# Kernel optimization log

Measured on AMD Instinct MI355X. Metric: run time of the kernel, lower is better.

The kernel has to match this reference:

```python
import jax, jax.numpy as jnp
import numpy as np

B, S, C = 2, 2048, 1536
HQ, HKV = 16, 4
DQK, DV = 128, 96
MAX_POS = 2048
CLIP = 5.0
EPS = 1e-5


def layer_norm(x, g, b):
    mu = jnp.mean(x, axis=-1, keepdims=True)
    var = jnp.mean(jnp.square(x - mu), axis=-1, keepdims=True)
    return (x - mu) * jax.lax.rsqrt(var + EPS) * g + b


def rms_bn(x, g, ms):
    # eval-mode EMA RMS batch-norm: per-channel running mean-square `ms`
    return x * jax.lax.rsqrt(ms + EPS) * g


def rope(x):
    # x: [B, S, H, C] with C even
    c = x.shape[-1]
    nf = c // 2
    s = x.shape[1]
    positions = jnp.arange(s, dtype=x.dtype)
    lin = jnp.arange(nf, dtype=x.dtype)
    end = max(MAX_POS - nf + 1.0, 1.0)
    geom = jnp.exp(jnp.linspace(0.0, jnp.log(jnp.asarray(end, dtype=x.dtype)), nf))
    inv_freq = 1.0 / (lin + geom)
    theta = positions[:, None] * inv_freq          # [S, nf]
    theta = jnp.repeat(theta, 2, axis=-1)[:, None, :]  # [S, 1, C]
    x_rot = jnp.stack([-x[..., 1::2], x[..., ::2]], axis=-1).reshape(x.shape)
    return x * jnp.cos(theta) + x_rot * jnp.sin(theta)


def setup_inputs() -> dict:
    key = jax.random.key(0)
    ks = jax.random.split(key, 8)
    d = {
        'x': jax.random.normal(ks[0], (B, S, C), dtype=jnp.float32),
        'bn1_g': jnp.ones((C,), jnp.float32),
        'bn1_ms': jnp.ones((C,), jnp.float32),
        'Wq': jax.random.normal(ks[1], (C, HQ * DQK), jnp.float32) * 0.02,
        'Wk': jax.random.normal(ks[2], (C, HKV * DQK), jnp.float32) * 0.02,
        'Wv': jax.random.normal(ks[3], (C, HKV * DV), jnp.float32) * 0.02,
        'qn_g': jnp.ones((DQK,), jnp.float32), 'qn_b': jnp.zeros((DQK,), jnp.float32),
        'kn_g': jnp.ones((DQK,), jnp.float32), 'kn_b': jnp.zeros((DQK,), jnp.float32),
        'vn_g': jnp.ones((DV,), jnp.float32), 'vn_b': jnp.zeros((DV,), jnp.float32),
        'Wo': jax.random.normal(ks[4], (HQ * DV, C), jnp.float32) * 0.02,
        'bo': jnp.zeros((C,), jnp.float32),
        'bn2_g': jnp.ones((C,), jnp.float32),
        'bn2_ms': jnp.ones((C,), jnp.float32),
    }
    return d


def reference(x, bn1_g, bn1_ms, Wq, Wk, Wv, qn_g, qn_b, kn_g, kn_b, vn_g, vn_b, Wo, bo, bn2_g, bn2_ms):
    rep = HQ // HKV
    h = rms_bn(x, bn1_g, bn1_ms)                       # [B,S,C]
    q = (h @ Wq).reshape(B, S, HQ, DQK)
    k = (h @ Wk).reshape(B, S, HKV, DQK)
    v = (h @ Wv).reshape(B, S, HKV, DV)
    q = layer_norm(q, qn_g, qn_b)
    k = layer_norm(k, kn_g, kn_b)
    v = layer_norm(v, vn_g, vn_b)
    q = rope(q)
    k = rope(k)
    # torch .repeat(1,1,rep,1) tiles head axis: [h0..hkv-1] * rep
    k = jnp.tile(k, (1, 1, rep, 1))                    # [B,S,HQ,DQK]
    v = jnp.tile(v, (1, 1, rep, 1))                    # [B,S,HQ,DV]
    logits = jnp.einsum('bshc,bShc->bhsS', q, k) / (DQK ** 0.5)
    logits = jnp.tanh(logits / CLIP) * CLIP
    attn = jax.nn.softmax(logits, axis=-1)
    y = jnp.einsum('bhsS,bShc->bshc', attn, v)         # [B,S,HQ,DV]
    y = y.reshape(B, S, HQ * DV)
    y = y @ Wo + bo
    y = rms_bn(y, bn2_g, bn2_ms)
    return y
```

## Files before the change

kernel.cpp:

```cpp
#include <hip/hip_runtime.h>
#include <hip/hip_bf16.h>
#include <math.h>

typedef __hip_bfloat16 bf16;
typedef __attribute__((ext_vector_type(8))) short short8;
typedef __attribute__((ext_vector_type(4))) short short4s;
typedef __attribute__((ext_vector_type(4))) float f32x4;

constexpr int Bb=2, Ss=2048, Cc=1536, HQn=16, HKVn=4, Dqk=128, Dv=96;
constexpr int NR   = Bb*Ss;
constexpr int NQKV = HQn*Dqk + HKVn*Dqk + HKVn*Dv;
constexpr int COL_K = HQn*Dqk;
constexpr int COL_V = COL_K + HKVn*Dqk;
constexpr int NY   = HQn*Dv;
constexpr float EPSf=1e-5f, CLIPf=5.0f;
constexpr float LOG2E = 1.44269504089f;

__device__ __forceinline__ float s2f(short s) {
    unsigned u = ((unsigned)(unsigned short)s) << 16;
    return __builtin_bit_cast(float, u);
}
__device__ __forceinline__ short f2s(float v) {
    bf16 b = __float2bfloat16(v);
    return __builtin_bit_cast(short, b);
}
__device__ __forceinline__ bool is_bf(const void* tagp) {
    return ((*(const unsigned*)tagp) & 0xFFFFu) != 0u;
}
__device__ __forceinline__ float ldd(const void* p, size_t i, bool bf) {
    return bf ? s2f(((const short*)p)[i]) : ((const float*)p)[i];
}
__device__ __forceinline__ void gll16(const void* src, void* lds) {
    __builtin_amdgcn_global_load_lds(
        (const __attribute__((address_space(1))) void*)src,
        (__attribute__((address_space(3))) void*)lds, 16, 0, 0);
}

__global__ __launch_bounds__(256) void k_pre(const void* g1, const void* ms1,
        const void* bo, const void* g2, const void* ms2,
        float* __restrict__ ascale, float* __restrict__ ebias,
        float* __restrict__ escale, float2* __restrict__ tab) {
    bool bf = is_bf(ms1);
    int idx = blockIdx.x*256 + threadIdx.x;
    if (idx < Cc) {
        ascale[idx] = rsqrtf(ldd(ms1,idx,bf) + EPSf) * ldd(g1,idx,bf);
        ebias[idx]  = ldd(bo,idx,bf);
        escale[idx] = rsqrtf(ldd(ms2,idx,bf) + EPSf) * ldd(g2,idx,bf);
    }
    if (idx < Ss*64) {
        int s = idx >> 6, f = idx & 63;
        float geom = expf((float)f * (logf(1985.0f) * (1.0f/63.0f)));
        float invf = 1.0f / ((float)f + geom);
        float th = (float)s * invf;
        tab[idx] = make_float2(cosf(th), sinf(th));
    }
}

__global__ __launch_bounds__(256) void k_bn1(const void* __restrict__ x,
        short* __restrict__ h, const void* tagp) {
    bool bf = is_bf(tagp);
    size_t i8 = (size_t)(blockIdx.x*256 + threadIdx.x) * 8;
    if (i8 >= (size_t)NR*Cc) return;
    if (bf) {
        *(short8*)(h + i8) = *(const short8*)((const short*)x + i8);
    } else {
        const float* xf = (const float*)x + i8;
        short8 o;
        #pragma unroll
        for (int j=0;j<8;++j) o[j] = f2s(xf[j]);
        *(short8*)(h + i8) = o;
    }
}

__global__ __launch_bounds__(256) void k_trw(const void* __restrict__ Wq,
        const void* __restrict__ Wk, const void* __restrict__ Wv,
        const void* __restrict__ Wo, short* __restrict__ WT,
        const float* __restrict__ ascale, const void* tagp) {
    __shared__ short tile[32][33];
    bool bf = is_bf(tagp);
    int gt = blockIdx.x*32;
    int k0 = blockIdx.y*32;
    const void* W; int N, nl;
    bool doscale = true;
    if      (gt < 2048) { W = Wq; N = 2048; nl = gt; }
    else if (gt < 2560) { W = Wk; N = 512;  nl = gt - 2048; }
    else if (gt < 2944) { W = Wv; N = 384;  nl = gt - 2560; }
    else                { W = Wo; N = 1536; nl = gt - 2944; doscale = false; }
    int t = threadIdx.x, c = t & 31;
    #pragma unroll
    for (int r8=0; r8<32; r8+=8) {
        int r = r8 + (t>>5);
        float sc = doscale ? ascale[k0+r] : 1.0f;
        tile[r][c] = f2s(ldd(W, (size_t)(k0+r)*N + nl + c, bf) * sc);
    }
    __syncthreads();
    #pragma unroll
    for (int r8=0; r8<32; r8+=8) {
        int r = r8 + (t>>5);
        WT[(size_t)(gt + r)*Cc + k0 + c] = tile[c][r];
    }
}

__global__ __launch_bounds__(256) void k_gemm(const short* __restrict__ A,
        const short* __restrict__ BT, void* __restrict__ Cout,
        int M, int N, int K,
        const float* __restrict__ ebias, const float* __restrict__ escale,
        int epi, const void* tagp) {
    __shared__ short As[128*32];
    __shared__ short Bs[128*32];
    const int t = threadIdx.x;
    const int w = t >> 6, lane = t & 63;
    const int l15 = lane & 15, quad = lane >> 4;
    const int wm = (w>>1)*64, wn = (w&1)*64;
    const int m0 = blockIdx.y*128, n0 = blockIdx.x*128;
    const int c0 = lane >> 2;
    const int koff = (lane & 3) * 8;

    f32x4 acc[4][4];
    #pragma unroll
    for (int i=0;i<4;++i)
        #pragma unroll
        for (int j=0;j<4;++j) acc[i][j] = (f32x4){0.f,0.f,0.f,0.f};

    for (int k0 = 0; k0 < K; k0 += 32) {
        __syncthreads();
        #pragma unroll
        for (int c=0; c<2; ++c) {
            int rA = w*32 + c*16;
            const short* ga = A  + (size_t)(m0 + rA + c0)*K + k0 + koff;
            const short* gb = BT + (size_t)(n0 + rA + c0)*K + k0 + koff;
            gll16(ga, &As[rA*32]);
            gll16(gb, &Bs[rA*32]);
        }
        __syncthreads();
        short8 af[4], bfr[4];
        #pragma unroll
        for (int mt=0; mt<4; ++mt)
            af[mt] = *(const short8*)&As[(wm + mt*16 + l15)*32 + quad*8];
        #pragma unroll
        for (int nt=0; nt<4; ++nt)
            bfr[nt] = *(const short8*)&Bs[(wn + nt*16 + l15)*32 + quad*8];
        #pragma unroll
        for (int mt=0; mt<4; ++mt)
            #pragma unroll
            for (int nt=0; nt<4; ++nt)
                acc[mt][nt] = __builtin_amdgcn_mfma_f32_16x16x32_bf16(
                    af[mt], bfr[nt], acc[mt][nt], 0, 0, 0);
    }

    const bool outf32 = epi && !is_bf(tagp);
    #pragma unroll
    for (int mt=0; mt<4; ++mt) {
        #pragma unroll
        for (int nt=0; nt<4; ++nt) {
            int col = n0 + wn + nt*16 + l15;
            float eb = epi ? ebias[col]  : 0.f;
            float es = epi ? escale[col] : 1.f;
            #pragma unroll
            for (int reg=0; reg<4; ++reg) {
                int row = m0 + wm + mt*16 + quad*4 + reg;
                float v = acc[mt][nt][reg];
                if (epi) v = (v + eb) * es;
                if (outf32) ((float*)Cout)[(size_t)row*N + col] = v;
                else        ((short*)Cout)[(size_t)row*N + col] = f2s(v);
            }
        }
    }
}

__global__ __launch_bounds__(512, 2) void k_gemm256(const short* __restrict__ A,
        const short* __restrict__ BT, short* __restrict__ Cout,
        int M, int Npad, int Nout, int K) {
    __shared__ __align__(16) short smem[4 * 2 * 256 * 32];
    const int t = threadIdx.x;
    const int w = t >> 6, lane = t & 63;
    const int wm = w >> 2, wn = w & 3;
    const int l15 = lane & 15, quad = lane >> 4;

    const int nwg = gridDim.x, cpx = nwg >> 3;
    const int swz = (blockIdx.x & 7)*cpx + (blockIdx.x >> 3);
    const int ntx = Npad >> 8;
    const int n0 = (swz % ntx) << 8, m0 = (swz / ntx) << 8;

    const int srow = lane >> 2;
    const int scol = (lane & 3) * 16;
    const short* Asrc = A  + (size_t)(m0 + srow)*K;
    const short* Bsrc = BT + (size_t)(n0 + srow)*K;

    f32x4 acc[8][4];
    #pragma unroll
    for (int i=0;i<8;++i)
        #pragma unroll
        for (int j=0;j<4;++j) acc[i][j] = (f32x4){0.f,0.f,0.f,0.f};

    const int H = K >> 5;
    auto stage = [&](int h) {
        const int slot = h & 3;
        char* AD = (char*)smem + slot*32768;
        char* BD = AD + 16384;
        const size_t koff = (size_t)h << 5;
        #pragma unroll
        for (int uu=0; uu<2; ++uu) {
            const int u = w + uu*8;
            const char* as = (const char*)(Asrc + (size_t)(u*16)*K + koff) + scol;
            const char* bs = (const char*)(Bsrc + (size_t)(u*16)*K + koff) + scol;
            gll16(as, AD + u*1024);
            gll16(bs, BD + u*1024);
        }
    };

    stage(0);
    if (H > 1) stage(1);
    if (H > 2) stage(2);

    for (int h = 0; h < H; ++h) {
        if (h+3 < H) stage(h+3);
        const int rem = H-1-h;
        if      (rem >= 3) asm volatile("s_waitcnt vmcnt(12)" ::: "memory");
        else if (rem == 2) asm volatile("s_waitcnt vmcnt(8)"  ::: "memory");
        else if (rem == 1) asm volatile("s_waitcnt vmcnt(4)"  ::: "memory");
        else               asm volatile("s_waitcnt vmcnt(0)"  ::: "memory");
        __builtin_amdgcn_s_barrier();

        const int slot = h & 3;
        const char* AD = (const char*)smem + slot*32768;
        const char* BD = AD + 16384;
        short8 af[8], bfr[4];
        #pragma unroll
        for (int i=0;i<8;++i) {
            int row = wm*128 + i*16 + l15;
            af[i] = *(const short8*)(AD + row*64 + quad*16);
        }
        #pragma unroll
        for (int j=0;j<4;++j) {
            int row = wn*64 + j*16 + l15;
            bfr[j] = *(const short8*)(BD + row*64 + quad*16);
        }
        asm volatile("s_waitcnt lgkmcnt(0)" ::: "memory");
        __builtin_amdgcn_sched_barrier(0);
        __builtin_amdgcn_s_setprio(1);
        #pragma unroll
        for (int i=0;i<8;++i)
            #pragma unroll
            for (int j=0;j<4;++j)
                acc[i][j] = __builtin_amdgcn_mfma_f32_16x16x32_bf16(
                    af[i], bfr[j], acc[i][j], 0, 0, 0);
        __builtin_amdgcn_s_setprio(0);
        __builtin_amdgcn_s_barrier();
    }

    #pragma unroll
    for (int mt=0; mt<8; ++mt) {
        #pragma unroll
        for (int nt=0; nt<4; ++nt) {
            int col = n0 + wn*64 + nt*16 + l15;
            if (col < Nout) {
                #pragma unroll
                for (int reg=0; reg<4; ++reg) {
                    int row = m0 + wm*128 + mt*16 + quad*4 + reg;
                    Cout[(size_t)row*Nout + col] = f2s(acc[mt][nt][reg]);
                }
            }
        }
    }
}

__global__ __launch_bounds__(256) void k_ln(short* __restrict__ qkvb,
        const float2* __restrict__ tab,
        const void* qg, const void* qb_, const void* kg, const void* kb_,
        const void* vg, const void* vb_, const void* tagp) {
    bool bf = is_bf(tagp);
    int R = blockIdx.x*4 + (threadIdx.x>>6);
    int lane = threadIdx.x & 63;
    int hidx = R % 24, bs = R / 24, s = bs % Ss;
    const void *g, *bia; int coff, D, dorope;
    if (hidx < 16)      { coff = hidx*Dqk;              D = Dqk; g = qg; bia = qb_; dorope = 1; }
    else if (hidx < 20) { coff = COL_K + (hidx-16)*Dqk; D = Dqk; g = kg; bia = kb_; dorope = 1; }
    else                { coff = COL_V + (hidx-20)*Dv;  D = Dv;  g = vg; bia = vb_; dorope = 0; }
    short* p = qkvb + (size_t)bs*NQKV + coff;
    int d0 = lane*2;
    bool act = d0 < D;
    float v0 = 0.f, v1 = 0.f;
    if (act) { v0 = s2f(p[d0]); v1 = s2f(p[d0+1]); }
    float sum = v0 + v1;
    #pragma unroll
    for (int m=1; m<64; m<<=1) sum += __shfl_xor(sum, m);
    float mu = sum / (float)D;
    float c0 = act ? v0-mu : 0.f, c1 = act ? v1-mu : 0.f;
    float sq = c0*c0 + c1*c1;
    #pragma unroll
    for (int m=1; m<64; m<<=1) sq += __shfl_xor(sq, m);
    float r = rsqrtf(sq/(float)D + EPSf);
    if (act) {
        float y0 = c0*r*ldd(g,d0,bf)   + ldd(bia,d0,bf);
        float y1 = c1*r*ldd(g,d0+1,bf) + ldd(bia,d0+1,bf);
        if (dorope) {
            float2 cs = tab[s*64 + lane];
            float t0 = y0*cs.x - y1*cs.y;
            y1 = y1*cs.x + y0*cs.y;
            y0 = t0;
        }
        p[d0] = f2s(y0); p[d0+1] = f2s(y1);
    }
}

__global__ __launch_bounds__(256) void k_trv(const short* __restrict__ qkvb,
        short* __restrict__ vT) {
    __shared__ short tile[32][33];
    int bs0 = blockIdx.x*32;
    int dg0 = blockIdx.y*32;
    int t = threadIdx.x, c = t & 31;
    #pragma unroll
    for (int r8=0; r8<32; r8+=8) {
        int r = r8 + (t>>5);
        tile[r][c] = qkvb[(size_t)(bs0+r)*NQKV + COL_V + dg0 + c];
    }
    __syncthreads();
    int b = bs0 >> 11, s0 = bs0 & 2047;
    int s = s0 + c;
    int sp = (s & ~63) + ((s>>5)&1)*32 + ((s>>2)&3)*8 + ((s>>4)&1)*4 + (s&3);
    #pragma unroll
    for (int r8=0; r8<32; r8+=8) {
        int r = r8 + (t>>5);
        vT[((size_t)(b*384 + dg0 + r))*Ss + sp] = tile[c][r];
    }
}

__global__ __launch_bounds__(512, 4) void k_attn(const short* __restrict__ qkvb,
        const short* __restrict__ vT, short* __restrict__ Yb) {
    __shared__ __align__(16) short smem[2*64*128 + 2*96*64];
    auto Ks  = (short(*)[64*128])smem;
    auto VTs = (short(*)[96*64])(smem + 2*64*128);
    const int wg = blockIdx.x;
    const int xcd = wg & 7, idx = wg >> 3;
    const int b = xcd >> 2, kvh = xcd & 3;
    const int qb = idx >> 2, hsub = idx & 3;
    const int hq = hsub*4 + kvh;
    const int q0 = qb*128;
    const int t = threadIdx.x;
    const int w = t >> 6, lane = t & 63;
    const int qw = w & 3, half = w >> 2;
    const int l15 = lane & 15, quad = lane >> 4;
    const int xr = (l15 & 7) * 16;
    const float ctan = 2.0f * (0.0883883476f / CLIPf) * LOG2E;
    const float c2   = -2.0f * CLIPf * LOG2E;

    const short* Kb = qkvb + ((size_t)b*Ss)*NQKV + COL_K + kvh*Dqk;
    const short* Vb = vT + ((size_t)(b*HKVn + kvh)*Dv)*Ss;

    const int rK = 4*w + (lane>>4);
    const char* kq0 = (const char*)Kb + (size_t)rK*NQKV*2
                    + (((lane&15)*16) ^ ((rK&7)*16));
    const int dv0 = 8*w + (lane>>3);
    const char* vq0 = (const char*)Vb + (size_t)dv0*Ss*2
                    + (((lane&7)*16) ^ ((dv0&7)*16));
    const size_t KADV = (size_t)64*NQKV*2;
    const size_t KOFF2 = (size_t)32*NQKV*2;
    const size_t VOFF2 = (size_t)64*Ss*2;

    auto issue_stage = [&](int pb) {
        char* KD = (char*)&Ks[pb][0];
        char* VD = (char*)&VTs[pb][0];
        gll16(kq0,         KD + w*1024);
        gll16(kq0 + KOFF2, KD + (w+8)*1024);
        gll16(vq0,         VD + w*1024);
        if (w < 4) gll16(vq0 + VOFF2, VD + (w+8)*1024);
        kq0 += KADV; vq0 += 128;
    };

    issue_stage(0);

    short8 qf[2][4];
    #pragma unroll
    for (int qt=0; qt<2; ++qt) {
        const short* qp = qkvb + (size_t)(b*Ss + q0 + qw*32 + qt*16 + l15)*NQKV + hq*Dqk;
        #pragma unroll
        for (int ds=0; ds<4; ++ds) qf[qt][ds] = *(const short8*)(qp + ds*32 + quad*8);
    }

    f32x4 oacc[2][6];
    #pragma unroll
    for (int qt=0; qt<2; ++qt)
        #pragma unroll
        for (int nt=0; nt<6; ++nt) oacc[qt][nt] = (f32x4){0.f,0.f,0.f,0.f};
    float lsum[2] = {0.f, 0.f};

    int p = 0;
    constexpr int NCH = Ss/64;
    for (int kc = 0; kc < NCH; ++kc) {
        __syncthreads();
        if (kc+1 < NCH) issue_stage(p^1);

        const char* KsB  = (const char*)&Ks[p][0];
        const char* VTsB = (const char*)&VTs[p][0];

        short8 pa[2];
        #pragma unroll
        for (int kt=0; kt<2; ++kt) {
            const int r = (half*2 + kt)*16 + l15;
            const char* krow = KsB + r*256;
            short8 kf[4];
            #pragma unroll
            for (int ds=0; ds<4; ++ds)
                kf[ds] = *(const short8*)(krow + ((ds*64 + quad*16) ^ xr));
            f32x4 s0 = (f32x4){0.f,0.f,0.f,0.f}, s1 = (f32x4){0.f,0.f,0.f,0.f};
            __builtin_amdgcn_s_setprio(1);
            #pragma unroll
            for (int ds=0; ds<4; ++ds) {
                s0 = __builtin_amdgcn_mfma_f32_16x16x32_bf16(kf[ds], qf[0][ds], s0, 0, 0, 0);
                s1 = __builtin_amdgcn_mfma_f32_16x16x32_bf16(kf[ds], qf[1][ds], s1, 0, 0, 0);
            }
            __builtin_amdgcn_s_setprio(0);
            #pragma unroll
            for (int j=0; j<4; ++j) {
                float u0 = __builtin_amdgcn_exp2f(s0[j] * ctan);
                float p0 = __builtin_amdgcn_exp2f(c2 * __builtin_amdgcn_rcpf(u0 + 1.0f));
                pa[0][kt*4+j] = f2s(p0); lsum[0] += p0;
                float u1 = __builtin_amdgcn_exp2f(s1[j] * ctan);
                float p1 = __builtin_amdgcn_exp2f(c2 * __builtin_amdgcn_rcpf(u1 + 1.0f));
                pa[1][kt*4+j] = f2s(p1); lsum[1] += p1;
            }
        }

        __builtin_amdgcn_s_setprio(1);
        #pragma unroll
        for (int nt=0; nt<6; ++nt) {
            const int dvrow = nt*16 + l15;
            short8 vf = *(const short8*)(VTsB + dvrow*128 + ((half*64 + quad*16) ^ xr));
            oacc[0][nt] = __builtin_amdgcn_mfma_f32_16x16x32_bf16(pa[0], vf, oacc[0][nt], 0, 0, 0);
            oacc[1][nt] = __builtin_amdgcn_mfma_f32_16x16x32_bf16(pa[1], vf, oacc[1][nt], 0, 0, 0);
        }
        __builtin_amdgcn_s_setprio(0);
        p ^= 1;
    }

    __syncthreads();
    float* red = (float*)smem;
    const int rbase = (qw*64 + lane)*53;
    if (half == 1) {
        #pragma unroll
        for (int qt=0; qt<2; ++qt)
            #pragma unroll
            for (int nt=0; nt<6; ++nt)
                *(f32x4*)&red[rbase + (qt*6+nt)*4] = oacc[qt][nt];
        red[rbase+48] = lsum[0];
        red[rbase+49] = lsum[1];
    }
    __syncthreads();
    if (half == 0) {
        #pragma unroll
        for (int qt=0; qt<2; ++qt)
            #pragma unroll
            for (int nt=0; nt<6; ++nt) {
                f32x4 o = *(const f32x4*)&red[rbase + (qt*6+nt)*4];
                #pragma unroll
                for (int j=0;j<4;++j) oacc[qt][nt][j] += o[j];
            }
        lsum[0] += red[rbase+48];
        lsum[1] += red[rbase+49];

        float lred[2];
        #pragma unroll
        for (int qt=0; qt<2; ++qt) {
            float l = lsum[qt];
            l += __shfl_xor(l, 16);
            l += __shfl_xor(l, 32);
            lred[qt] = l;
        }
        #pragma unroll
        for (int qt=0; qt<2; ++qt) {
            float rinv[4];
            #pragma unroll
            for (int reg=0; reg<4; ++reg)
                rinv[reg] = __builtin_amdgcn_rcpf(__shfl(lred[qt], quad*4 + reg, 16));
            #pragma unroll
            for (int nt=0; nt<6; ++nt)
                #pragma unroll
                for (int reg=0; reg<4; ++reg) {
                    int row = q0 + qw*32 + qt*16 + quad*4 + reg;
                    Yb[(size_t)(b*Ss + row)*NY + hq*Dv + nt*16 + l15] =
                        f2s(oacc[qt][nt][reg] * rinv[reg]);
                }
        }
    }
}

extern "C" void kernel_launch(void* const* d_in, const int* in_sizes, int n_in,
                              void* d_out, int out_size, void* d_ws, size_t ws_size,
                              hipStream_t stream) {
    const void* x     = d_in[0];
    const void* bn1g  = d_in[1];
    const void* bn1ms = d_in[2];
    const void* Wq    = d_in[3];
    const void* Wk    = d_in[4];
    const void* Wv    = d_in[5];
    const void* qng   = d_in[6];
    const void* qnb   = d_in[7];
    const void* kng   = d_in[8];
    const void* knb   = d_in[9];
    const void* vng   = d_in[10];
    const void* vnb   = d_in[11];
    const void* Wo    = d_in[12];
    const void* bo    = d_in[13];
    const void* bn2g  = d_in[14];
    const void* bn2ms = d_in[15];

    char* wsb = (char*)d_ws;
    float*  ascale = (float*)(wsb);
    float*  ebias  = (float*)(wsb + 6144);
    float*  escale = (float*)(wsb + 12288);
    float2* tab    = (float2*)(wsb + 18432);
    short*  h      = (short*)(wsb + 1067520);
    short*  WT     = (short*)(wsb + 13650432);
    short*  qkv    = (short*)(wsb + 27412992);
    short*  vT     = (short*)(wsb + 51530240);
    short*  y      = (short*)(wsb + 54675968);
    short*  WoT    = WT + (size_t)NQKV*Cc;

    k_pre<<<512, 256, 0, stream>>>(bn1g, bn1ms, bo, bn2g, bn2ms,
                                   ascale, ebias, escale, tab);

    const short* Agemm;
    if (in_sizes && in_sizes[0] == (int)((size_t)NR*Cc*2)) {
        Agemm = (const short*)x;
    } else {
        k_bn1<<<(NR*Cc/8 + 255)/256, 256, 0, stream>>>(x, h, bn1ms);
        Agemm = h;
    }

    k_trw<<<dim3(4480/32, Cc/32), 256, 0, stream>>>(Wq, Wk, Wv, Wo, WT, ascale, bn1ms);

    k_gemm256<<<dim3(192), 512, 0, stream>>>(Agemm, WT, qkv, NR, 3072, NQKV, Cc);

    k_ln<<<NR*24/4, 256, 0, stream>>>(qkv, tab, qng, qnb, kng, knb, vng, vnb, bn1ms);
    k_trv<<<dim3(NR/32, 384/32), 256, 0, stream>>>(qkv, vT);

    k_attn<<<512, 512, 0, stream>>>(qkv, vT, y);

    k_gemm<<<dim3(Cc/128, NR/128), 256, 0, stream>>>(
        y, WoT, d_out, NR, Cc, NY, ebias, escale, 1, bn1ms);
}
```

Measured before the change: 335.8 us.

## Triple-buffer output projection GEMM with async loads and swizzled block order

Replaces the single-buffered output-projection GEMM with a version that keeps a three-slot LDS ring. Global-to-LDS loads are issued two K-steps ahead and paced with explicit vmcnt waits, so memory latency overlaps with MFMA work instead of stalling at every barrier. Workgroups are launched on a 1D grid remapped in groups of eight to improve L2 reuse, and MFMA priority is raised during the compute phase. In exchange it uses more shared memory per block, which caps occupancy at three blocks per CU, and it depends on hand-tuned waitcnt counts.

```diff
diff --git a/kernel.cpp b/kernel.cpp
--- a/kernel.cpp
+++ b/kernel.cpp
@@ -101,73 +101,6 @@
     }
 }
 
-__global__ __launch_bounds__(256) void k_gemm(const short* __restrict__ A,
-        const short* __restrict__ BT, void* __restrict__ Cout,
-        int M, int N, int K,
-        const float* __restrict__ ebias, const float* __restrict__ escale,
-        int epi, const void* tagp) {
-    __shared__ short As[128*32];
-    __shared__ short Bs[128*32];
-    const int t = threadIdx.x;
-    const int w = t >> 6, lane = t & 63;
-    const int l15 = lane & 15, quad = lane >> 4;
-    const int wm = (w>>1)*64, wn = (w&1)*64;
-    const int m0 = blockIdx.y*128, n0 = blockIdx.x*128;
-    const int c0 = lane >> 2;
-    const int koff = (lane & 3) * 8;
-
-    f32x4 acc[4][4];
-    #pragma unroll
-    for (int i=0;i<4;++i)
-        #pragma unroll
-        for (int j=0;j<4;++j) acc[i][j] = (f32x4){0.f,0.f,0.f,0.f};
-
-    for (int k0 = 0; k0 < K; k0 += 32) {
-        __syncthreads();
-        #pragma unroll
-        for (int c=0; c<2; ++c) {
-            int rA = w*32 + c*16;
-            const short* ga = A  + (size_t)(m0 + rA + c0)*K + k0 + koff;
-            const short* gb = BT + (size_t)(n0 + rA + c0)*K + k0 + koff;
-            gll16(ga, &As[rA*32]);
-            gll16(gb, &Bs[rA*32]);
-        }
-        __syncthreads();
-        short8 af[4], bfr[4];
-        #pragma unroll
-        for (int mt=0; mt<4; ++mt)
-            af[mt] = *(const short8*)&As[(wm + mt*16 + l15)*32 + quad*8];
-        #pragma unroll
-        for (int nt=0; nt<4; ++nt)
-            bfr[nt] = *(const short8*)&Bs[(wn + nt*16 + l15)*32 + quad*8];
-        #pragma unroll
-        for (int mt=0; mt<4; ++mt)
-            #pragma unroll
-            for (int nt=0; nt<4; ++nt)
-                acc[mt][nt] = __builtin_amdgcn_mfma_f32_16x16x32_bf16(
-                    af[mt], bfr[nt], acc[mt][nt], 0, 0, 0);
-    }
-
-    const bool outf32 = epi && !is_bf(tagp);
-    #pragma unroll
-    for (int mt=0; mt<4; ++mt) {
-        #pragma unroll
-        for (int nt=0; nt<4; ++nt) {
-            int col = n0 + wn + nt*16 + l15;
-            float eb = epi ? ebias[col]  : 0.f;
-            float es = epi ? escale[col] : 1.f;
-            #pragma unroll
-            for (int reg=0; reg<4; ++reg) {
-                int row = m0 + wm + mt*16 + quad*4 + reg;
-                float v = acc[mt][nt][reg];
-                if (epi) v = (v + eb) * es;
-                if (outf32) ((float*)Cout)[(size_t)row*N + col] = v;
-                else        ((short*)Cout)[(size_t)row*N + col] = f2s(v);
-            }
-        }
-    }
-}
-
 __global__ __launch_bounds__(512, 2) void k_gemm256(const short* __restrict__ A,
         const short* __restrict__ BT, short* __restrict__ Cout,
         int M, int Npad, int Nout, int K) {
@@ -260,6 +193,105 @@
                     int row = m0 + wm*128 + mt*16 + quad*4 + reg;
                     Cout[(size_t)row*Nout + col] = f2s(acc[mt][nt][reg]);
                 }
+            }
+        }
+    }
+}
+
+__global__ __launch_bounds__(256, 3) void k_gemmo(const short* __restrict__ A,
+        const short* __restrict__ BT, void* __restrict__ Cout,
+        int M, int N, int K,
+        const float* __restrict__ ebias, const float* __restrict__ escale,
+        const void* tagp) {
+    __shared__ __align__(16) short smem[3 * 2 * 128 * 32];
+    const int t = threadIdx.x;
+    const int w = t >> 6, lane = t & 63;
+    const int wm = w >> 1, wn = w & 1;
+    const int l15 = lane & 15, quad = lane >> 4;
+
+    const int nwg = gridDim.x, cpx = nwg >> 3;
+    const int swz = (blockIdx.x & 7)*cpx + (blockIdx.x >> 3);
+    const int ntx = N >> 7;
+    const int n0 = (swz % ntx) << 7, m0 = (swz / ntx) << 7;
+
+    const int srow = lane >> 2;
+    const int scol = (lane & 3) * 16;
+    const short* Asrc = A  + (size_t)(m0 + srow)*K;
+    const short* Bsrc = BT + (size_t)(n0 + srow)*K;
+
+    f32x4 acc[4][4];
+    #pragma unroll
+    for (int i=0;i<4;++i)
+        #pragma unroll
+        for (int j=0;j<4;++j) acc[i][j] = (f32x4){0.f,0.f,0.f,0.f};
+
+    const int H = K >> 5;
+    auto stage = [&](int h) {
+        const int slot = h % 3;
+        char* AD = (char*)smem + slot*16384;
+        char* BD = AD + 8192;
+        const size_t koff = (size_t)h << 5;
+        #pragma unroll
+        for (int uu=0; uu<2; ++uu) {
+            const int u = w + uu*4;
+            const char* as = (const char*)(Asrc + (size_t)(u*16)*K + koff) + scol;
+            const char* bs = (const char*)(Bsrc + (size_t)(u*16)*K + koff) + scol;
+            gll16(as, AD + u*1024);
+            gll16(bs, BD + u*1024);
+        }
+    };
+
+    stage(0);
+    if (H > 1) stage(1);
+
+    for (int h = 0; h < H; ++h) {
+        if (h+2 < H) stage(h+2);
+        const int rem = H-1-h;
+        if      (rem >= 2) asm volatile("s_waitcnt vmcnt(8)" ::: "memory");
+        else if (rem == 1) asm volatile("s_waitcnt vmcnt(4)" ::: "memory");
+        else               asm volatile("s_waitcnt vmcnt(0)" ::: "memory");
+        __builtin_amdgcn_s_barrier();
+
+        const int slot = h % 3;
+        const char* AD = (const char*)smem + slot*16384;
+        const char* BD = AD + 8192;
+        short8 af[4], bfr[4];
+        #pragma unroll
+        for (int i=0;i<4;++i) {
+            int row = wm*64 + i*16 + l15;
+            af[i] = *(const short8*)(AD + row*64 + quad*16);
+        }
+        #pragma unroll
+        for (int j=0;j<4;++j) {
+            int row = wn*64 + j*16 + l15;
+            bfr[j] = *(const short8*)(BD + row*64 + quad*16);
+        }
+        asm volatile("s_waitcnt lgkmcnt(0)" ::: "memory");
+        __builtin_amdgcn_sched_barrier(0);
+        __builtin_amdgcn_s_setprio(1);
+        #pragma unroll
+        for (int i=0;i<4;++i)
+            #pragma unroll
+            for (int j=0;j<4;++j)
+                acc[i][j] = __builtin_amdgcn_mfma_f32_16x16x32_bf16(
+                    af[i], bfr[j], acc[i][j], 0, 0, 0);
+        __builtin_amdgcn_s_setprio(0);
+        __builtin_amdgcn_s_barrier();
+    }
+
+    const bool outf32 = !is_bf(tagp);
+    #pragma unroll
+    for (int mt=0; mt<4; ++mt) {
+        #pragma unroll
+        for (int nt=0; nt<4; ++nt) {
+            int col = n0 + wn*64 + nt*16 + l15;
+            float eb = ebias[col], es = escale[col];
+            #pragma unroll
+            for (int reg=0; reg<4; ++reg) {
+                int row = m0 + wm*64 + mt*16 + quad*4 + reg;
+                float v = (acc[mt][nt][reg] + eb) * es;
+                if (outf32) ((float*)Cout)[(size_t)row*N + col] = v;
+                else        ((short*)Cout)[(size_t)row*N + col] = f2s(v);
             }
         }
     }
@@ -537,6 +569,6 @@
 
     k_attn<<<512, 512, 0, stream>>>(qkv, vT, y);
 
-    k_gemm<<<dim3(Cc/128, NR/128), 256, 0, stream>>>(
-        y, WoT, d_out, NR, Cc, NY, ebias, escale, 1, bn1ms);
-}
+    k_gemmo<<<dim3((NR/128)*(Cc/128)), 256, 0, stream>>>(
+        y, WoT, d_out, NR, Cc, NY, ebias, escale, bn1ms);
+}
```

Measured after the change: 321.5 us. 4.3% less time.
